# Kernel optimization log

Measured on AMD Instinct MI355X. Metric: run time of the kernel, lower is better.

Reference implementation:

```python
import jax, jax.numpy as jnp
import numpy as np


def setup_inputs() -> dict:
    key = jax.random.key(0)
    k1, k2 = jax.random.split(key)
    B, T, S, D = 8, 1024, 1024, 2048
    support_sets = jax.random.normal(k1, (B, S, D), dtype=jnp.float32)
    X_hats = jax.random.normal(k2, (B, T, D), dtype=jnp.float32)
    return {"support_sets": support_sets, "X_hats": X_hats}


def reference(support_sets, X_hats):
    # Pairwise cosine similarity: out[b, t, s] = cos(X_hats[b, t], support_sets[b, s])
    # Matches torch.nn.functional.cosine_similarity with eps=1e-10:
    #   dot / max(||x|| * ||y||, eps)
    eps = 1e-10
    x_norm = jnp.linalg.norm(X_hats, axis=-1)          # [B, T]
    s_norm = jnp.linalg.norm(support_sets, axis=-1)    # [B, S]
    dots = jnp.einsum('btd,bsd->bts', X_hats, support_sets)  # [B, T, S]
    denom = jnp.maximum(x_norm[:, :, None] * s_norm[:, None, :], eps)
    return dots / denom
```

## Files before the change

### kernel.cpp

```cpp
#include <hip/hip_runtime.h>
#include <hip/hip_bf16.h>

typedef __attribute__((ext_vector_type(4))) float        f32x4;
typedef __attribute__((ext_vector_type(8))) short        s16x8;
typedef __attribute__((ext_vector_type(4))) unsigned int u32x4;
typedef __attribute__((ext_vector_type(2))) unsigned int u32x2;

#define Bb 8
#define Tt 1024
#define Ss 1024
#define Dd 2048
#define BM 128
#define BN 128
#define BK 64

__device__ __forceinline__ unsigned pack2_bf16(float f0, float f1) {
  unsigned u0 = __builtin_bit_cast(unsigned, f0) + 0x8000u;
  unsigned u1 = __builtin_bit_cast(unsigned, f1) + 0x8000u;
  return (u0 >> 16) | (u1 & 0xffff0000u);
}

__device__ __forceinline__ void gld_lds16(const void* g, void* l) {
  __builtin_amdgcn_global_load_lds(
      (__attribute__((address_space(1))) void*)(void*)(g),
      (__attribute__((address_space(3))) void*)l, 16, 0, 0);
}

__global__ __launch_bounds__(256, 4)
void convert_kernel(const float* __restrict__ sup, const float* __restrict__ xh,
                    unsigned* __restrict__ abf, unsigned* __restrict__ bbf,
                    float* __restrict__ invA, float* __restrict__ invB)
{
  const int wave = threadIdx.x >> 6, lane = threadIdx.x & 63;
  const int rowg = (blockIdx.x * 4 + wave) * 2;
  const float* src; unsigned* dst; float* inv; int row;
  if (rowg < 8192) { row = rowg;         src = xh;  dst = abf; inv = invA; }
  else             { row = rowg - 8192;  src = sup; dst = bbf; inv = invB; }

  const f32x4* s0 = (const f32x4*)(src + (size_t)row * Dd);
  const f32x4* s1 = (const f32x4*)(src + (size_t)(row + 1) * Dd);

  f32x4 v0[8], v1[8];
  #pragma unroll
  for (int j = 0; j < 8; ++j) v0[j] = s0[j * 64 + lane];
  #pragma unroll
  for (int j = 0; j < 8; ++j) v1[j] = s1[j * 64 + lane];
  __builtin_amdgcn_sched_barrier(0);

  u32x2* d0 = (u32x2*)(dst + (size_t)row * (Dd / 2));
  u32x2* d1 = (u32x2*)(dst + (size_t)(row + 1) * (Dd / 2));
  float sq0 = 0.0f, sq1 = 0.0f;
  #pragma unroll
  for (int j = 0; j < 8; ++j) {
    f32x4 a = v0[j];
    sq0 = fmaf(a[0], a[0], fmaf(a[1], a[1], fmaf(a[2], a[2], fmaf(a[3], a[3], sq0))));
    d0[j * 64 + lane] = (u32x2){pack2_bf16(a[0], a[1]), pack2_bf16(a[2], a[3])};
  }
  #pragma unroll
  for (int j = 0; j < 8; ++j) {
    f32x4 a = v1[j];
    sq1 = fmaf(a[0], a[0], fmaf(a[1], a[1], fmaf(a[2], a[2], fmaf(a[3], a[3], sq1))));
    d1[j * 64 + lane] = (u32x2){pack2_bf16(a[0], a[1]), pack2_bf16(a[2], a[3])};
  }

  #pragma unroll
  for (int m = 32; m; m >>= 1) { sq0 += __shfl_xor(sq0, m, 64); sq1 += __shfl_xor(sq1, m, 64); }
  if (lane == 0) { inv[row] = 1.0f / sqrtf(sq0); inv[row + 1] = 1.0f / sqrtf(sq1); }
}

__global__ __launch_bounds__(256, 2)
void gemm_kernel(const short* __restrict__ abf, const short* __restrict__ bbf,
                 const float* __restrict__ invA, const float* __restrict__ invB,
                 float* __restrict__ out)
{
  __shared__ short As[2][BM * BK];
  __shared__ short Bs[2][BN * BK];

  const int bid0 = blockIdx.x;
  const int bid  = ((bid0 & 7) << 6) | (bid0 >> 3);
  const int b    = bid >> 6;
  const int tile = bid & 63;
  const int tm   = tile >> 3;
  const int tn   = tile & 7;

  const int t = threadIdx.x, wave = t >> 6, lane = t & 63;

  const int srow = lane >> 3;
  const int cph  = lane & 7;
  const int r0   = wave * 32;

  const size_t aRow = (size_t)(b * Tt + tm * BM);
  const size_t bRow = (size_t)(b * Ss + tn * BN);
  const short *gA0, *gA1, *gA2, *gA3, *gB0, *gB1, *gB2, *gB3;
  {
    int r;
    r = r0 + 0 * 8 + srow; gA0 = abf + (aRow + r) * Dd + (cph ^ (r & 7)) * 8;
                           gB0 = bbf + (bRow + r) * Dd + (cph ^ (r & 7)) * 8;
    r = r0 + 1 * 8 + srow; gA1 = abf + (aRow + r) * Dd + (cph ^ (r & 7)) * 8;
                           gB1 = bbf + (bRow + r) * Dd + (cph ^ (r & 7)) * 8;
    r = r0 + 2 * 8 + srow; gA2 = abf + (aRow + r) * Dd + (cph ^ (r & 7)) * 8;
                           gB2 = bbf + (bRow + r) * Dd + (cph ^ (r & 7)) * 8;
    r = r0 + 3 * 8 + srow; gA3 = abf + (aRow + r) * Dd + (cph ^ (r & 7)) * 8;
                           gB3 = bbf + (bRow + r) * Dd + (cph ^ (r & 7)) * 8;
  }

  const int wm = (wave >> 1) << 6;
  const int wn = (wave & 1) << 6;
  const int lm = lane & 15;
  const int kq = lane >> 4;

  f32x4 acc[4][4];
  #pragma unroll
  for (int i = 0; i < 4; ++i)
    #pragma unroll
    for (int j = 0; j < 4; ++j)
      acc[i][j] = (f32x4)0.0f;

#define STAGE(bi) do {                                                   \
    gld_lds16(gA0, As[bi] + (r0 + 0)  * BK);                             \
    gld_lds16(gA1, As[bi] + (r0 + 8)  * BK);                             \
    gld_lds16(gA2, As[bi] + (r0 + 16) * BK);                             \
    gld_lds16(gA3, As[bi] + (r0 + 24) * BK);                             \
    gld_lds16(gB0, Bs[bi] + (r0 + 0)  * BK);                             \
    gld_lds16(gB1, Bs[bi] + (r0 + 8)  * BK);                             \
    gld_lds16(gB2, Bs[bi] + (r0 + 16) * BK);                             \
    gld_lds16(gB3, Bs[bi] + (r0 + 24) * BK);                             \
    gA0 += BK; gA1 += BK; gA2 += BK; gA3 += BK;                          \
    gB0 += BK; gB1 += BK; gB2 += BK; gB3 += BK;                          \
  } while (0)

#define COMPUTE(bi) do {                                                 \
    _Pragma("unroll")                                                    \
    for (int ks = 0; ks < 2; ++ks) {                                     \
      const int pchunk = ((ks * 4 + kq) ^ (lm & 7)) * 8;                 \
      s16x8 af[4], bfr[4];                                               \
      _Pragma("unroll")                                                  \
      for (int i = 0; i < 4; ++i) {                                      \
        af[i]  = *(const s16x8*)(As[bi] + (wm + i * 16 + lm) * BK + pchunk); \
        bfr[i] = *(const s16x8*)(Bs[bi] + (wn + i * 16 + lm) * BK + pchunk); \
      }                                                                  \
      _Pragma("unroll")                                                  \
      for (int mi = 0; mi < 4; ++mi)                                     \
        _Pragma("unroll")                                                \
        for (int ni = 0; ni < 4; ++ni)                                   \
          acc[mi][ni] = __builtin_amdgcn_mfma_f32_16x16x32_bf16(af[mi], bfr[ni], acc[mi][ni], 0, 0, 0); \
    }                                                                    \
  } while (0)

  STAGE(0);
  __syncthreads();

  for (int k0 = 0; k0 < Dd; k0 += 2 * BK) {
    STAGE(1);
    COMPUTE(0);
    __syncthreads();
    if (k0 + 2 * BK < Dd) STAGE(0);
    COMPUTE(1);
    __syncthreads();
  }
#undef STAGE
#undef COMPUTE

  const float* iA = invA + b * Tt + tm * BM;
  const float* iB = invB + b * Ss + tn * BN;
  float* outb = out + (size_t)(b * Tt + tm * BM) * Ss + tn * BN;
  const int m0 = wm + kq * 4;
  const int n0 = wn + lm;
  #pragma unroll
  for (int mi = 0; mi < 4; ++mi) {
    #pragma unroll
    for (int r = 0; r < 4; ++r) {
      const int mrow = m0 + mi * 16 + r;
      const float ia = iA[mrow];
      float* orow = outb + (size_t)mrow * Ss;
      #pragma unroll
      for (int ni = 0; ni < 4; ++ni) {
        const int ncol = n0 + ni * 16;
        orow[ncol] = acc[mi][ni][r] * (ia * iB[ncol]);
      }
    }
  }
}

#define LDKF 40
#define BKF 32
__global__ __launch_bounds__(256, 2)
void paircos_kernel(const float* __restrict__ sup, const float* __restrict__ xh,
                    float* __restrict__ out)
{
  __shared__ short As[BM * LDKF];
  __shared__ short Bs[BN * LDKF];
  __shared__ float invA[BM];
  __shared__ float invB[BN];

  const int bid = blockIdx.x;
  const int b = bid >> 6, tile = bid & 63, tm = tile >> 3, tn = tile & 7;
  const float* Abase = xh  + (size_t)(b * Tt + tm * BM) * Dd;
  const float* Bbase = sup + (size_t)(b * Ss + tn * BN) * Dd;
  const int t = threadIdx.x, row = t >> 1, kh = t & 1;
  const f32x4* agp = (const f32x4*)(Abase + (size_t)row * Dd + kh * 16);
  const f32x4* bgp = (const f32x4*)(Bbase + (size_t)row * Dd + kh * 16);
  u32x4* awr = (u32x4*)(As + row * LDKF + kh * 16);
  u32x4* bwr = (u32x4*)(Bs + row * LDKF + kh * 16);
  const int wave = t >> 6, lane = t & 63;
  const int wm = (wave >> 1) << 6, wn = (wave & 1) << 6;
  const int lm = lane & 15, kq = lane >> 4;

  f32x4 acc[4][4];
  #pragma unroll
  for (int i = 0; i < 4; ++i)
    #pragma unroll
    for (int j = 0; j < 4; ++j) acc[i][j] = (f32x4)0.0f;
  float sqa = 0.0f, sqb = 0.0f;
  f32x4 areg[4], breg[4];
  #pragma unroll
  for (int i = 0; i < 4; ++i) { areg[i] = agp[i]; breg[i] = bgp[i]; }

  for (int k0 = 0; k0 < Dd; k0 += BKF) {
    unsigned pa[8], pb[8];
    #pragma unroll
    for (int i = 0; i < 4; ++i) {
      sqa = fmaf(areg[i][0], areg[i][0], sqa); sqa = fmaf(areg[i][1], areg[i][1], sqa);
      sqa = fmaf(areg[i][2], areg[i][2], sqa); sqa = fmaf(areg[i][3], areg[i][3], sqa);
      pa[i*2+0] = pack2_bf16(areg[i][0], areg[i][1]); pa[i*2+1] = pack2_bf16(areg[i][2], areg[i][3]);
      sqb = fmaf(breg[i][0], breg[i][0], sqb); sqb = fmaf(breg[i][1], breg[i][1], sqb);
      sqb = fmaf(breg[i][2], breg[i][2], sqb); sqb = fmaf(breg[i][3], breg[i][3], sqb);
      pb[i*2+0] = pack2_bf16(breg[i][0], breg[i][1]); pb[i*2+1] = pack2_bf16(breg[i][2], breg[i][3]);
    }
    __syncthreads();
    awr[0] = (u32x4){pa[0],pa[1],pa[2],pa[3]}; awr[1] = (u32x4){pa[4],pa[5],pa[6],pa[7]};
    bwr[0] = (u32x4){pb[0],pb[1],pb[2],pb[3]}; bwr[1] = (u32x4){pb[4],pb[5],pb[6],pb[7]};
    __syncthreads();
    if (k0 + BKF < Dd) {
      const int off = (k0 + BKF) >> 2;
      #pragma unroll
      for (int i = 0; i < 4; ++i) { areg[i] = agp[off + i]; breg[i] = bgp[off + i]; }
    }
    s16x8 af[4], bfr[4];
    #pragma unroll
    for (int i = 0; i < 4; ++i) {
      af[i]  = *(const s16x8*)(As + (wm + i*16 + lm) * LDKF + kq * 8);
      bfr[i] = *(const s16x8*)(Bs + (wn + i*16 + lm) * LDKF + kq * 8);
    }
    #pragma unroll
    for (int mi = 0; mi < 4; ++mi)
      #pragma unroll
      for (int ni = 0; ni < 4; ++ni)
        acc[mi][ni] = __builtin_amdgcn_mfma_f32_16x16x32_bf16(af[mi], bfr[ni], acc[mi][ni], 0, 0, 0);
  }
  __syncthreads();
  ((float*)As)[t] = sqa; ((float*)Bs)[t] = sqb;
  __syncthreads();
  if (t < 128) {
    invA[t] = 1.0f / sqrtf(((float*)As)[2*t] + ((float*)As)[2*t+1]);
    invB[t] = 1.0f / sqrtf(((float*)Bs)[2*t] + ((float*)Bs)[2*t+1]);
  }
  __syncthreads();
  float* outb = out + (size_t)(b * Tt + tm * BM) * Ss + tn * BN;
  const int m0 = wm + kq * 4, n0 = wn + lm;
  #pragma unroll
  for (int mi = 0; mi < 4; ++mi) {
    #pragma unroll
    for (int r = 0; r < 4; ++r) {
      const int mrow = m0 + mi * 16 + r;
      const float ia = invA[mrow];
      float* orow = outb + (size_t)mrow * Ss;
      #pragma unroll
      for (int ni = 0; ni < 4; ++ni) {
        const int ncol = n0 + ni * 16;
        orow[ncol] = acc[mi][ni][r] * (ia * invB[ncol]);
      }
    }
  }
}

extern "C" void kernel_launch(void* const* d_in, const int* in_sizes, int n_in,
                              void* d_out, int out_size, void* d_ws, size_t ws_size,
                              hipStream_t stream) {
  const float* sup = (const float*)d_in[0];
  const float* xh  = (const float*)d_in[1];
  float* out = (float*)d_out;

  const size_t nElem = (size_t)Bb * Tt * Dd;
  const size_t bfBytes = nElem * sizeof(short);
  const size_t NEED = 2 * bfBytes + 2 * (size_t)Bb * Tt * sizeof(float);

  if (ws_size >= NEED) {
    unsigned* abf = (unsigned*)d_ws;
    unsigned* bbf = (unsigned*)((char*)d_ws + bfBytes);
    float* invA = (float*)((char*)d_ws + 2 * bfBytes);
    float* invB = invA + (size_t)Bb * Tt;
    convert_kernel<<<dim3(2048), dim3(256), 0, stream>>>(sup, xh, abf, bbf, invA, invB);
    gemm_kernel<<<dim3(512), dim3(256), 0, stream>>>((const short*)abf, (const short*)bbf,
                                                     invA, invB, out);
  } else {
    paircos_kernel<<<dim3(512), dim3(256), 0, stream>>>(sup, xh, out);
  }
}
```

Baseline: 199.3 us.

## Keep two GEMM stages in flight with vmcnt waits; split convert into per-row blocks

The GEMM main loop now issues both LDS stages up front. It then waits with s_waitcnt vmcnt(8) plus a raw barrier, so one stage's global-to-LDS loads stay in flight while the other stage computes. This replaces the full __syncthreads drains. The convert kernel is restructured to one block per row with an LDS reduction, and is launched twice, once per input. Correctness depends on the vmcnt count matching the number of loads each STAGE issues per thread, and the extra launch adds overhead.

```diff
diff --git a/kernel.cpp b/kernel.cpp
--- a/kernel.cpp
+++ b/kernel.cpp
@@ -26,46 +26,30 @@
       (__attribute__((address_space(3))) void*)l, 16, 0, 0);
 }
 
-__global__ __launch_bounds__(256, 4)
-void convert_kernel(const float* __restrict__ sup, const float* __restrict__ xh,
-                    unsigned* __restrict__ abf, unsigned* __restrict__ bbf,
-                    float* __restrict__ invA, float* __restrict__ invB)
+__global__ __launch_bounds__(256, 8)
+void convert_kernel(const float* __restrict__ src, unsigned* __restrict__ dst,
+                    float* __restrict__ inv)
 {
-  const int wave = threadIdx.x >> 6, lane = threadIdx.x & 63;
-  const int rowg = (blockIdx.x * 4 + wave) * 2;
-  const float* src; unsigned* dst; float* inv; int row;
-  if (rowg < 8192) { row = rowg;         src = xh;  dst = abf; inv = invA; }
-  else             { row = rowg - 8192;  src = sup; dst = bbf; inv = invB; }
-
-  const f32x4* s0 = (const f32x4*)(src + (size_t)row * Dd);
-  const f32x4* s1 = (const f32x4*)(src + (size_t)(row + 1) * Dd);
-
-  f32x4 v0[8], v1[8];
-  #pragma unroll
-  for (int j = 0; j < 8; ++j) v0[j] = s0[j * 64 + lane];
-  #pragma unroll
-  for (int j = 0; j < 8; ++j) v1[j] = s1[j * 64 + lane];
-  __builtin_amdgcn_sched_barrier(0);
-
-  u32x2* d0 = (u32x2*)(dst + (size_t)row * (Dd / 2));
-  u32x2* d1 = (u32x2*)(dst + (size_t)(row + 1) * (Dd / 2));
-  float sq0 = 0.0f, sq1 = 0.0f;
-  #pragma unroll
-  for (int j = 0; j < 8; ++j) {
-    f32x4 a = v0[j];
-    sq0 = fmaf(a[0], a[0], fmaf(a[1], a[1], fmaf(a[2], a[2], fmaf(a[3], a[3], sq0))));
-    d0[j * 64 + lane] = (u32x2){pack2_bf16(a[0], a[1]), pack2_bf16(a[2], a[3])};
-  }
-  #pragma unroll
-  for (int j = 0; j < 8; ++j) {
-    f32x4 a = v1[j];
-    sq1 = fmaf(a[0], a[0], fmaf(a[1], a[1], fmaf(a[2], a[2], fmaf(a[3], a[3], sq1))));
-    d1[j * 64 + lane] = (u32x2){pack2_bf16(a[0], a[1]), pack2_bf16(a[2], a[3])};
-  }
-
-  #pragma unroll
-  for (int m = 32; m; m >>= 1) { sq0 += __shfl_xor(sq0, m, 64); sq1 += __shfl_xor(sq1, m, 64); }
-  if (lane == 0) { inv[row] = 1.0f / sqrtf(sq0); inv[row + 1] = 1.0f / sqrtf(sq1); }
+  __shared__ float red[4];
+  const int row = blockIdx.x;
+  const int t = threadIdx.x;
+  const f32x4* s = (const f32x4*)(src + (size_t)row * Dd);
+  const f32x4 a = s[t];
+  const f32x4 b = s[256 + t];
+
+  float sq = fmaf(a[0], a[0], fmaf(a[1], a[1], fmaf(a[2], a[2], a[3] * a[3])));
+  sq = fmaf(b[0], b[0], fmaf(b[1], b[1], fmaf(b[2], b[2], fmaf(b[3], b[3], sq))));
+
+  u32x2* d = (u32x2*)(dst + (size_t)row * (Dd / 2));
+  d[t]       = (u32x2){pack2_bf16(a[0], a[1]), pack2_bf16(a[2], a[3])};
+  d[256 + t] = (u32x2){pack2_bf16(b[0], b[1]), pack2_bf16(b[2], b[3])};
+
+  #pragma unroll
+  for (int m = 32; m; m >>= 1) sq += __shfl_xor(sq, m, 64);
+  const int wave = t >> 6, lane = t & 63;
+  if (lane == 0) red[wave] = sq;
+  __syncthreads();
+  if (t == 0) inv[row] = 1.0f / sqrtf(red[0] + red[1] + red[2] + red[3]);
 }
 
 __global__ __launch_bounds__(256, 2)
@@ -147,19 +131,35 @@
     }                                                                    \
   } while (0)
 
+#define WAIT_BAR(n) do {                                                 \
+    asm volatile("s_waitcnt vmcnt(" #n ")" ::: "memory");                \
+    __builtin_amdgcn_s_barrier();                                        \
+    __builtin_amdgcn_sched_barrier(0);                                   \
+  } while (0)
+
   STAGE(0);
-  __syncthreads();
-
-  for (int k0 = 0; k0 < Dd; k0 += 2 * BK) {
+  STAGE(1);
+
+  for (int i = 0; i < 15; ++i) {
+    WAIT_BAR(8);
+    COMPUTE(0);
+    __builtin_amdgcn_sched_barrier(0);
+    __builtin_amdgcn_s_barrier();
+    STAGE(0);
+    WAIT_BAR(8);
+    COMPUTE(1);
+    __builtin_amdgcn_sched_barrier(0);
+    __builtin_amdgcn_s_barrier();
     STAGE(1);
-    COMPUTE(0);
-    __syncthreads();
-    if (k0 + 2 * BK < Dd) STAGE(0);
-    COMPUTE(1);
-    __syncthreads();
-  }
+  }
+
+  WAIT_BAR(8);
+  COMPUTE(0);
+  WAIT_BAR(0);
+  COMPUTE(1);
 #undef STAGE
 #undef COMPUTE
+#undef WAIT_BAR
 
   const float* iA = invA + b * Tt + tm * BM;
   const float* iB = invB + b * Ss + tn * BN;
@@ -290,7 +290,8 @@
     unsigned* bbf = (unsigned*)((char*)d_ws + bfBytes);
     float* invA = (float*)((char*)d_ws + 2 * bfBytes);
     float* invB = invA + (size_t)Bb * Tt;
-    convert_kernel<<<dim3(2048), dim3(256), 0, stream>>>(sup, xh, abf, bbf, invA, invB);
+    convert_kernel<<<dim3(8192), dim3(256), 0, stream>>>(xh, abf, invA);
+    convert_kernel<<<dim3(8192), dim3(256), 0, stream>>>(sup, bbf, invB);
     gemm_kernel<<<dim3(512), dim3(256), 0, stream>>>((const short*)abf, (const short*)bbf,
                                                      invA, invB, out);
   } else {
```

Measured after the change: 193.1 us. 3.1% less time.
